# Kernel tuning notes

Measured on AMD Instinct MI355X. Metric: run time of the kernel, lower is better.

Reference implementation:

```python
import jax, jax.numpy as jnp
import numpy as np

EMB = 1024
HEAD = 64

def setup_inputs() -> dict:
    key = jax.random.key(0)
    kx, kq, kk, kv = jax.random.split(key, 4)
    x = jax.random.normal(kx, (8, 2048, EMB), dtype=jnp.float32)
    # nn.Linear(emb, head, bias=False): y = x @ W.T, W: [head, emb]. Store as [emb, head].
    s = 1.0 / np.sqrt(EMB)
    Wq = jax.random.uniform(kq, (EMB, HEAD), jnp.float32, -s, s)
    Wk = jax.random.uniform(kk, (EMB, HEAD), jnp.float32, -s, s)
    Wv = jax.random.uniform(kv, (EMB, HEAD), jnp.float32, -s, s)
    return {"x": x, "Wq": Wq, "Wk": Wk, "Wv": Wv}

def reference(x, Wq, Wk, Wv):
    B, T, C = x.shape
    q = x @ Wq  # [B,T,H]
    k = x @ Wk
    v = x @ Wv
    # NOTE: original scales by emb_size C, not head_size.
    wei = jnp.einsum('bth,bsh->bts', q, k) / jnp.sqrt(jnp.asarray(C, x.dtype))
    causal = jnp.tril(jnp.ones((T, T), dtype=bool))
    wei = jnp.where(causal, wei, -jnp.inf)
    wei = jax.nn.softmax(wei, axis=-1)
    return jnp.einsum('bts,bsh->bth', wei, v)
```

## Files before the change

kernel.cpp:

```cpp
#include <hip/hip_runtime.h>
#include <hip/hip_bf16.h>

typedef __bf16 bf16_t;
typedef __bf16 bf16x8 __attribute__((ext_vector_type(8)));
typedef __bf16 bf16x4 __attribute__((ext_vector_type(4)));
typedef float  f32x4  __attribute__((ext_vector_type(4)));

#define MFMA_BF16(A, B, C) __builtin_amdgcn_mfma_f32_16x16x32_bf16((A), (B), (C), 0, 0, 0)

#define BATCH 8
#define SEQ   2048
#define EMB   1024
#define HEAD  64

typedef __attribute__((address_space(3))) void as3_void;
typedef const __attribute__((address_space(1))) void as1_void;
#define GLOAD_LDS16(g, l) \
  __builtin_amdgcn_global_load_lds((as1_void*)(g), (as3_void*)(l), 16, 0, 0)

__global__ __launch_bounds__(256) void wtrans_kernel(
    const float* __restrict__ Wq, const float* __restrict__ Wk,
    const float* __restrict__ Wv, bf16_t* __restrict__ WT)
{
  __shared__ float tile[64][65];
  const int m  = blockIdx.x >> 4;
  const int kt = blockIdx.x & 15;
  const float* W = (m == 0) ? Wq : (m == 1) ? Wk : Wv;
  const float scale = (m == 0) ? 0.03125f : 1.0f;
  const int k0 = kt * 64;

  #pragma unroll
  for (int i = 0; i < 16; ++i) {
    int idx = i * 256 + threadIdx.x;
    int kk = idx >> 6, n = idx & 63;
    tile[kk][n] = W[(size_t)(k0 + kk) * HEAD + n];
  }
  __syncthreads();
  #pragma unroll
  for (int i = 0; i < 16; ++i) {
    int idx = i * 256 + threadIdx.x;
    int n = idx >> 6, kk = idx & 63;
    WT[((size_t)m * HEAD + n) * EMB + k0 + kk] = (bf16_t)(tile[kk][n] * scale);
  }
}

#define A_BYTES 8192
#define B_BYTES 12288
#define BUF_BYTES 20480

__global__ __launch_bounds__(256, 2) void qkv_kernel(
    const float* __restrict__ x, const bf16_t* __restrict__ WT,
    bf16_t* __restrict__ qo, bf16_t* __restrict__ ko, bf16_t* __restrict__ vT)
{
  __shared__ char lds[4 * BUF_BYTES];

  const int tid  = threadIdx.x;
  const int lane = tid & 63;
  const int wave = tid >> 6;
  const int l15 = lane & 15, l4 = lane >> 4;
  const int wm = wave >> 1, wn = wave & 1;
  const int rowbase = blockIdx.x * 64;

  const int a_row_sub = lane >> 3;
  const int a_src_off = (((lane & 7) ^ a_row_sub) << 4);
  const int b_row_sub = lane >> 2;
  const int b_src_off = (lane & 3) * 16;

  const int aswz = (l15 & 7) << 4;

  f32x4 acc[2][6];
  #pragma unroll
  for (int m = 0; m < 2; ++m)
    #pragma unroll
    for (int n = 0; n < 6; ++n) acc[m][n] = (f32x4){0.f, 0.f, 0.f, 0.f};

#define STAGE(t)                                                               \
  {                                                                            \
    char* buf = lds + ((t) & 3) * BUF_BYTES;                                   \
    _Pragma("unroll")                                                          \
    for (int j = 0; j < 2; ++j) {                                              \
      const int g = wave * 2 + j;                                              \
      const int row = 8 * g + a_row_sub;                                       \
      const char* src = (const char*)x + (size_t)(rowbase + row) * 4096        \
                        + (size_t)(t) * 128 + a_src_off;                       \
      GLOAD_LDS16(src, buf + g * 1024);                                        \
    }                                                                          \
    _Pragma("unroll")                                                          \
    for (int j = 0; j < 3; ++j) {                                              \
      const int g = wave * 3 + j;                                              \
      const int row = 16 * g + b_row_sub;                                      \
      const char* src = (const char*)WT + (size_t)row * 2048                   \
                        + (size_t)(t) * 64 + b_src_off;                        \
      GLOAD_LDS16(src, buf + A_BYTES + g * 1024);                              \
    }                                                                          \
  }

#define COMPUTE(t)                                                             \
  {                                                                            \
    const char* Ab = lds + ((t) & 3) * BUF_BYTES;                              \
    const char* Bb = Ab + A_BYTES;                                             \
    bf16x8 afr[2];                                                             \
    _Pragma("unroll")                                                          \
    for (int m = 0; m < 2; ++m) {                                              \
      const int R = wm * 32 + m * 16 + l15;                                    \
      f32x4 p0 = *(const f32x4*)(Ab + R * 128 + ((l4 * 32) ^ aswz));           \
      f32x4 p1 = *(const f32x4*)(Ab + R * 128 + ((l4 * 32 + 16) ^ aswz));      \
      bf16x8 a;                                                                \
      a[0] = (bf16_t)p0.x; a[1] = (bf16_t)p0.y;                                \
      a[2] = (bf16_t)p0.z; a[3] = (bf16_t)p0.w;                                \
      a[4] = (bf16_t)p1.x; a[5] = (bf16_t)p1.y;                                \
      a[6] = (bf16_t)p1.z; a[7] = (bf16_t)p1.w;                                \
      afr[m] = a;                                                              \
    }                                                                          \
    _Pragma("unroll")                                                          \
    for (int n = 0; n < 6; ++n) {                                              \
      const int R = wn * 96 + n * 16 + l15;                                    \
      bf16x8 b = *(const bf16x8*)(Bb + R * 64 + l4 * 16);                      \
      acc[0][n] = MFMA_BF16(afr[0], b, acc[0][n]);                             \
      acc[1][n] = MFMA_BF16(afr[1], b, acc[1][n]);                             \
    }                                                                          \
  }

  STAGE(0); STAGE(1); STAGE(2);
  asm volatile("s_waitcnt vmcnt(10)" ::: "memory");
  __builtin_amdgcn_s_barrier();

  #pragma unroll 4
  for (int t = 0; t < 28; ++t) {
    COMPUTE(t);
    STAGE(t + 3);
    asm volatile("s_waitcnt vmcnt(10)" ::: "memory");
    __builtin_amdgcn_s_barrier();
  }
  COMPUTE(28); STAGE(31);
  asm volatile("s_waitcnt vmcnt(10)" ::: "memory");
  __builtin_amdgcn_s_barrier();
  COMPUTE(29);
  asm volatile("s_waitcnt vmcnt(5)" ::: "memory");
  __builtin_amdgcn_s_barrier();
  COMPUTE(30);
  asm volatile("s_waitcnt vmcnt(0)" ::: "memory");
  __builtin_amdgcn_s_barrier();
  COMPUTE(31);
#undef STAGE
#undef COMPUTE

  #pragma unroll
  for (int n = 0; n < 6; ++n) {
    const int col = wn * 96 + n * 16;
    #pragma unroll
    for (int m = 0; m < 2; ++m) {
      const int r0 = rowbase + wm * 32 + m * 16 + l4 * 4;
      if (col < 64) {
        #pragma unroll
        for (int i = 0; i < 4; ++i)
          qo[(size_t)(r0 + i) * HEAD + col + l15] = (bf16_t)acc[m][n][i];
      } else if (col < 128) {
        #pragma unroll
        for (int i = 0; i < 4; ++i)
          ko[(size_t)(r0 + i) * HEAD + col - 64 + l15] = (bf16_t)acc[m][n][i];
      } else {
        const int h = col - 128 + l15;
        bf16x4 pk;
        #pragma unroll
        for (int i = 0; i < 4; ++i) pk[i] = (bf16_t)acc[m][n][i];
        *(bf16x4*)(vT + ((size_t)(r0 >> 11) * HEAD + h) * SEQ + (r0 & 2047)) = pk;
      }
    }
  }
}

__global__ __launch_bounds__(512, 4) void attn_kernel(
    const bf16_t* __restrict__ q, const bf16_t* __restrict__ k,
    const bf16_t* __restrict__ vT, float* __restrict__ out)
{
  __shared__ bf16_t P[8][16][72];
  __shared__ float olds[8][16][68];
  __shared__ float lsums[8][16];
  const int lane = threadIdx.x & 63;
  const int wave = threadIdx.x >> 6;
  const int l15 = lane & 15, l4 = lane >> 4;
  const int batch = blockIdx.x & 7;
  const int pair  = blockIdx.x >> 3;
  const int strip = (wave < 4) ? pair : (127 - pair);
  const int wsub  = wave & 3;
  const int qrow  = strip * 16;

  const bf16_t* qb = q  + ((size_t)batch * SEQ + qrow) * HEAD;
  const bf16_t* kb = k  + (size_t)batch * SEQ * HEAD;
  const bf16_t* vb = vT + (size_t)batch * HEAD * SEQ;

  bf16x8 aq0 = *(const bf16x8*)(qb + (size_t)l15 * HEAD + l4 * 8);
  bf16x8 aq1 = *(const bf16x8*)(qb + (size_t)l15 * HEAD + 32 + l4 * 8);

  f32x4 o[4];
  #pragma unroll
  for (int i = 0; i < 4; ++i) o[i] = (f32x4){0.f, 0.f, 0.f, 0.f};
  float lsum[4] = {0.f, 0.f, 0.f, 0.f};

  const int ntiles = (qrow >> 6) + 1;
  for (int t = wsub; t < ntiles; t += 4) {
    const int kv0 = t * 64;

    bf16x8 v0[4], v1[4];
    #pragma unroll
    for (int nf = 0; nf < 4; ++nf) {
      const bf16_t* vp = vb + (size_t)(nf * 16 + l15) * SEQ + kv0 + l4 * 8;
      v0[nf] = *(const bf16x8*)vp;
      v1[nf] = *(const bf16x8*)(vp + 32);
    }

    f32x4 s[4];
    #pragma unroll
    for (int nf = 0; nf < 4; ++nf) s[nf] = (f32x4){0.f, 0.f, 0.f, 0.f};
    __builtin_amdgcn_s_setprio(1);
    #pragma unroll
    for (int nf = 0; nf < 4; ++nf) {
      const bf16_t* kp = kb + (size_t)(kv0 + nf * 16 + l15) * HEAD + l4 * 8;
      bf16x8 b0 = *(const bf16x8*)kp;
      bf16x8 b1 = *(const bf16x8*)(kp + 32);
      s[nf] = MFMA_BF16(aq0, b0, s[nf]);
      s[nf] = MFMA_BF16(aq1, b1, s[nf]);
    }
    __builtin_amdgcn_s_setprio(0);

    const bool diag = (t == ntiles - 1);
    #pragma unroll
    for (int nf = 0; nf < 4; ++nf) {
      #pragma unroll
      for (int i = 0; i < 4; ++i) {
        float e = __expf(s[nf][i]);
        if (diag) {
          const int col = kv0 + nf * 16 + l15;
          const int row = qrow + l4 * 4 + i;
          e = (col <= row) ? e : 0.f;
        }
        lsum[i] += e;
        P[wave][l4 * 4 + i][nf * 16 + l15] = (bf16_t)e;
      }
    }
    asm volatile("s_waitcnt lgkmcnt(0)" ::: "memory");

    bf16x8 ap0 = *(const bf16x8*)&P[wave][l15][l4 * 8];
    bf16x8 ap1 = *(const bf16x8*)&P[wave][l15][32 + l4 * 8];
    __builtin_amdgcn_s_setprio(1);
    #pragma unroll
    for (int nf = 0; nf < 4; ++nf) {
      o[nf] = MFMA_BF16(ap0, v0[nf], o[nf]);
      o[nf] = MFMA_BF16(ap1, v1[nf], o[nf]);
    }
    __builtin_amdgcn_s_setprio(0);
  }

  #pragma unroll
  for (int i = 0; i < 4; ++i) {
    float v = lsum[i];
    v += __shfl_xor(v, 1);
    v += __shfl_xor(v, 2);
    v += __shfl_xor(v, 4);
    v += __shfl_xor(v, 8);
    if (l15 == 0) lsums[wave][l4 * 4 + i] = v;
  }
  #pragma unroll
  for (int nf = 0; nf < 4; ++nf)
    #pragma unroll
    for (int i = 0; i < 4; ++i)
      olds[wave][l4 * 4 + i][nf * 16 + l15] = o[nf][i];
  __syncthreads();

  {
    const int g  = threadIdx.x >> 8;
    const int tt = threadIdx.x & 255;
    const int r = tt >> 4, c0 = tt & 15;
    const int sstrip = g ? (127 - pair) : pair;
    const int w0 = g * 4;
    const float s = lsums[w0][r] + lsums[w0+1][r] + lsums[w0+2][r] + lsums[w0+3][r];
    const float rinv = 1.0f / s;
    float* ob = out + ((size_t)batch * SEQ + sstrip * 16 + r) * HEAD;
    #pragma unroll
    for (int j = 0; j < 4; ++j) {
      const int c = c0 + 16 * j;
      float v = olds[w0][r][c] + olds[w0+1][r][c] + olds[w0+2][r][c] + olds[w0+3][r][c];
      ob[c] = v * rinv;
    }
  }
}

extern "C" void kernel_launch(void* const* d_in, const int* in_sizes, int n_in,
                              void* d_out, int out_size, void* d_ws, size_t ws_size,
                              hipStream_t stream)
{
  const float* x  = (const float*)d_in[0];
  const float* Wq = (const float*)d_in[1];
  const float* Wk = (const float*)d_in[2];
  const float* Wv = (const float*)d_in[3];
  float* out = (float*)d_out;

  const size_t SZ_QKV = (size_t)BATCH * SEQ * HEAD * sizeof(bf16_t);
  if (ws_size < 3 * SZ_QKV + (size_t)192 * EMB * sizeof(bf16_t)) return;
  char* ws = (char*)d_ws;
  bf16_t* qo = (bf16_t*)(ws);
  bf16_t* ko = (bf16_t*)(ws + SZ_QKV);
  bf16_t* vT = (bf16_t*)(ws + 2 * SZ_QKV);
  bf16_t* WT = (bf16_t*)(ws + 3 * SZ_QKV);

  wtrans_kernel<<<dim3(48),  dim3(256), 0, stream>>>(Wq, Wk, Wv, WT);
  qkv_kernel  <<<dim3(256), dim3(256), 0, stream>>>(x, WT, qo, ko, vT);
  attn_kernel <<<dim3(512), dim3(512), 0, stream>>>(qo, ko, vT, out);
}
```

Before: 56.81 us.

## Halve QKV row tile and balance attention KV tiles across all eight waves

The QKV projection now uses 32-row blocks launched as 512 blocks, with each wave owning 48 output columns, so more blocks are available to fill the CUs. The attention kernel pools the KV tiles of the paired short and long strips and deals them round-robin to all eight waves, replacing the fixed four waves per strip. This balances work inside the block at the cost of two reduction passes. The Q scale now folds in log2(e) so exp2f replaces __expf, V loads are moved after the softmax, and attention launch bounds drop to 2 blocks per SIMD minimum.

New measurement: 64.96 us. 14.4% more time.

```diff
diff --git a/kernel.cpp b/kernel.cpp
--- a/kernel.cpp
+++ b/kernel.cpp
@@ -26,7 +26,7 @@
   const int m  = blockIdx.x >> 4;
   const int kt = blockIdx.x & 15;
   const float* W = (m == 0) ? Wq : (m == 1) ? Wk : Wv;
-  const float scale = (m == 0) ? 0.03125f : 1.0f;
+  const float scale = (m == 0) ? 0.045084219f : 1.0f;
   const int k0 = kt * 64;
 
   #pragma unroll
@@ -44,9 +44,9 @@
   }
 }
 
-#define A_BYTES 8192
+#define A_BYTES 4096
 #define B_BYTES 12288
-#define BUF_BYTES 20480
+#define BUF_BYTES 16384
 
 __global__ __launch_bounds__(256, 2) void qkv_kernel(
     const float* __restrict__ x, const bf16_t* __restrict__ WT,
@@ -58,8 +58,7 @@
   const int lane = tid & 63;
   const int wave = tid >> 6;
   const int l15 = lane & 15, l4 = lane >> 4;
-  const int wm = wave >> 1, wn = wave & 1;
-  const int rowbase = blockIdx.x * 64;
+  const int rowbase = blockIdx.x * 32;
 
   const int a_row_sub = lane >> 3;
   const int a_src_off = (((lane & 7) ^ a_row_sub) << 4);
@@ -68,22 +67,20 @@
 
   const int aswz = (l15 & 7) << 4;
 
-  f32x4 acc[2][6];
+  f32x4 acc[2][3];
   #pragma unroll
   for (int m = 0; m < 2; ++m)
     #pragma unroll
-    for (int n = 0; n < 6; ++n) acc[m][n] = (f32x4){0.f, 0.f, 0.f, 0.f};
+    for (int n = 0; n < 3; ++n) acc[m][n] = (f32x4){0.f, 0.f, 0.f, 0.f};
 
 #define STAGE(t)                                                               \
   {                                                                            \
     char* buf = lds + ((t) & 3) * BUF_BYTES;                                   \
-    _Pragma("unroll")                                                          \
-    for (int j = 0; j < 2; ++j) {                                              \
-      const int g = wave * 2 + j;                                              \
-      const int row = 8 * g + a_row_sub;                                       \
+    {                                                                          \
+      const int row = 8 * wave + a_row_sub;                                    \
       const char* src = (const char*)x + (size_t)(rowbase + row) * 4096        \
                         + (size_t)(t) * 128 + a_src_off;                       \
-      GLOAD_LDS16(src, buf + g * 1024);                                        \
+      GLOAD_LDS16(src, buf + wave * 1024);                                     \
     }                                                                          \
     _Pragma("unroll")                                                          \
     for (int j = 0; j < 3; ++j) {                                              \
@@ -102,7 +99,7 @@
     bf16x8 afr[2];                                                             \
     _Pragma("unroll")                                                          \
     for (int m = 0; m < 2; ++m) {                                              \
-      const int R = wm * 32 + m * 16 + l15;                                    \
+      const int R = m * 16 + l15;                                              \
       f32x4 p0 = *(const f32x4*)(Ab + R * 128 + ((l4 * 32) ^ aswz));           \
       f32x4 p1 = *(const f32x4*)(Ab + R * 128 + ((l4 * 32 + 16) ^ aswz));      \
       bf16x8 a;                                                                \
@@ -113,8 +110,8 @@
       afr[m] = a;                                                              \
     }                                                                          \
     _Pragma("unroll")                                                          \
-    for (int n = 0; n < 6; ++n) {                                              \
-      const int R = wn * 96 + n * 16 + l15;                                    \
+    for (int n = 0; n < 3; ++n) {                                              \
+      const int R = wave * 48 + n * 16 + l15;                                  \
       bf16x8 b = *(const bf16x8*)(Bb + R * 64 + l4 * 16);                      \
       acc[0][n] = MFMA_BF16(afr[0], b, acc[0][n]);                             \
       acc[1][n] = MFMA_BF16(afr[1], b, acc[1][n]);                             \
@@ -122,21 +119,18 @@
   }
 
   STAGE(0); STAGE(1); STAGE(2);
-  asm volatile("s_waitcnt vmcnt(10)" ::: "memory");
+  asm volatile("s_waitcnt vmcnt(8)" ::: "memory");
   __builtin_amdgcn_s_barrier();
 
   #pragma unroll 4
-  for (int t = 0; t < 28; ++t) {
+  for (int t = 0; t < 29; ++t) {
     COMPUTE(t);
     STAGE(t + 3);
-    asm volatile("s_waitcnt vmcnt(10)" ::: "memory");
+    asm volatile("s_waitcnt vmcnt(8)" ::: "memory");
     __builtin_amdgcn_s_barrier();
   }
-  COMPUTE(28); STAGE(31);
-  asm volatile("s_waitcnt vmcnt(10)" ::: "memory");
-  __builtin_amdgcn_s_barrier();
   COMPUTE(29);
-  asm volatile("s_waitcnt vmcnt(5)" ::: "memory");
+  asm volatile("s_waitcnt vmcnt(4)" ::: "memory");
   __builtin_amdgcn_s_barrier();
   COMPUTE(30);
   asm volatile("s_waitcnt vmcnt(0)" ::: "memory");
@@ -146,11 +140,11 @@
 #undef COMPUTE
 
   #pragma unroll
-  for (int n = 0; n < 6; ++n) {
-    const int col = wn * 96 + n * 16;
+  for (int n = 0; n < 3; ++n) {
+    const int col = wave * 48 + n * 16;
     #pragma unroll
     for (int m = 0; m < 2; ++m) {
-      const int r0 = rowbase + wm * 32 + m * 16 + l4 * 4;
+      const int r0 = rowbase + m * 16 + l4 * 4;
       if (col < 64) {
         #pragma unroll
         for (int i = 0; i < 4; ++i)
@@ -170,7 +164,7 @@
   }
 }
 
-__global__ __launch_bounds__(512, 4) void attn_kernel(
+__global__ __launch_bounds__(512, 2) void attn_kernel(
     const bf16_t* __restrict__ q, const bf16_t* __restrict__ k,
     const bf16_t* __restrict__ vT, float* __restrict__ out)
 {
@@ -182,33 +176,38 @@
   const int l15 = lane & 15, l4 = lane >> 4;
   const int batch = blockIdx.x & 7;
   const int pair  = blockIdx.x >> 3;
-  const int strip = (wave < 4) ? pair : (127 - pair);
-  const int wsub  = wave & 3;
-  const int qrow  = strip * 16;
-
-  const bf16_t* qb = q  + ((size_t)batch * SEQ + qrow) * HEAD;
+  const int stripA = pair, stripB = 127 - pair;
+  const int nA = (stripA >> 2) + 1;
+  const int nB = (stripB >> 2) + 1;
+  const int ntot = nA + nB;
+
   const bf16_t* kb = k  + (size_t)batch * SEQ * HEAD;
   const bf16_t* vb = vT + (size_t)batch * HEAD * SEQ;
-
-  bf16x8 aq0 = *(const bf16x8*)(qb + (size_t)l15 * HEAD + l4 * 8);
-  bf16x8 aq1 = *(const bf16x8*)(qb + (size_t)l15 * HEAD + 32 + l4 * 8);
-
-  f32x4 o[4];
-  #pragma unroll
-  for (int i = 0; i < 4; ++i) o[i] = (f32x4){0.f, 0.f, 0.f, 0.f};
-  float lsum[4] = {0.f, 0.f, 0.f, 0.f};
-
-  const int ntiles = (qrow >> 6) + 1;
-  for (int t = wsub; t < ntiles; t += 4) {
-    const int kv0 = t * 64;
-
-    bf16x8 v0[4], v1[4];
-    #pragma unroll
-    for (int nf = 0; nf < 4; ++nf) {
-      const bf16_t* vp = vb + (size_t)(nf * 16 + l15) * SEQ + kv0 + l4 * 8;
-      v0[nf] = *(const bf16x8*)vp;
-      v1[nf] = *(const bf16x8*)(vp + 32);
-    }
+  const bf16_t* qbA = q + ((size_t)batch * SEQ + stripA * 16) * HEAD;
+  const bf16_t* qbB = q + ((size_t)batch * SEQ + stripB * 16) * HEAD;
+
+  const bf16x8 aqA0 = *(const bf16x8*)(qbA + (size_t)l15 * HEAD + l4 * 8);
+  const bf16x8 aqA1 = *(const bf16x8*)(qbA + (size_t)l15 * HEAD + 32 + l4 * 8);
+  const bf16x8 aqB0 = *(const bf16x8*)(qbB + (size_t)l15 * HEAD + l4 * 8);
+  const bf16x8 aqB1 = *(const bf16x8*)(qbB + (size_t)l15 * HEAD + 32 + l4 * 8);
+
+  f32x4 oA[4], oB[4];
+  #pragma unroll
+  for (int i = 0; i < 4; ++i) {
+    oA[i] = (f32x4){0.f, 0.f, 0.f, 0.f};
+    oB[i] = (f32x4){0.f, 0.f, 0.f, 0.f};
+  }
+  float lsA[4] = {0.f, 0.f, 0.f, 0.f};
+  float lsB[4] = {0.f, 0.f, 0.f, 0.f};
+
+  for (int i = wave; i < ntot; i += 8) {
+    const bool isA = (i < nA);
+    const int tile = isA ? i : (i - nA);
+    const int nS   = isA ? nA : nB;
+    const int qrow = (isA ? stripA : stripB) * 16;
+    const int kv0  = tile * 64;
+    const bf16x8 aq0 = isA ? aqA0 : aqB0;
+    const bf16x8 aq1 = isA ? aqA1 : aqB1;
 
     f32x4 s[4];
     #pragma unroll
@@ -224,65 +223,91 @@
     }
     __builtin_amdgcn_s_setprio(0);
 
-    const bool diag = (t == ntiles - 1);
+    const bool diag = (tile == nS - 1);
+    float tsum[4] = {0.f, 0.f, 0.f, 0.f};
     #pragma unroll
     for (int nf = 0; nf < 4; ++nf) {
       #pragma unroll
-      for (int i = 0; i < 4; ++i) {
-        float e = __expf(s[nf][i]);
+      for (int i2 = 0; i2 < 4; ++i2) {
+        float e = exp2f(s[nf][i2]);
         if (diag) {
           const int col = kv0 + nf * 16 + l15;
-          const int row = qrow + l4 * 4 + i;
+          const int row = qrow + l4 * 4 + i2;
           e = (col <= row) ? e : 0.f;
         }
-        lsum[i] += e;
-        P[wave][l4 * 4 + i][nf * 16 + l15] = (bf16_t)e;
-      }
+        tsum[i2] += e;
+        P[wave][l4 * 4 + i2][nf * 16 + l15] = (bf16_t)e;
+      }
+    }
+
+    bf16x8 v0[4], v1[4];
+    #pragma unroll
+    for (int nf = 0; nf < 4; ++nf) {
+      const bf16_t* vp = vb + (size_t)(nf * 16 + l15) * SEQ + kv0 + l4 * 8;
+      v0[nf] = *(const bf16x8*)vp;
+      v1[nf] = *(const bf16x8*)(vp + 32);
     }
     asm volatile("s_waitcnt lgkmcnt(0)" ::: "memory");
 
     bf16x8 ap0 = *(const bf16x8*)&P[wave][l15][l4 * 8];
     bf16x8 ap1 = *(const bf16x8*)&P[wave][l15][32 + l4 * 8];
     __builtin_amdgcn_s_setprio(1);
-    #pragma unroll
-    for (int nf = 0; nf < 4; ++nf) {
-      o[nf] = MFMA_BF16(ap0, v0[nf], o[nf]);
-      o[nf] = MFMA_BF16(ap1, v1[nf], o[nf]);
+    if (isA) {
+      #pragma unroll
+      for (int nf = 0; nf < 4; ++nf) {
+        oA[nf] = MFMA_BF16(ap0, v0[nf], oA[nf]);
+        oA[nf] = MFMA_BF16(ap1, v1[nf], oA[nf]);
+      }
+      #pragma unroll
+      for (int i2 = 0; i2 < 4; ++i2) lsA[i2] += tsum[i2];
+    } else {
+      #pragma unroll
+      for (int nf = 0; nf < 4; ++nf) {
+        oB[nf] = MFMA_BF16(ap0, v0[nf], oB[nf]);
+        oB[nf] = MFMA_BF16(ap1, v1[nf], oB[nf]);
+      }
+      #pragma unroll
+      for (int i2 = 0; i2 < 4; ++i2) lsB[i2] += tsum[i2];
     }
     __builtin_amdgcn_s_setprio(0);
   }
 
   #pragma unroll
-  for (int i = 0; i < 4; ++i) {
-    float v = lsum[i];
-    v += __shfl_xor(v, 1);
-    v += __shfl_xor(v, 2);
-    v += __shfl_xor(v, 4);
-    v += __shfl_xor(v, 8);
-    if (l15 == 0) lsums[wave][l4 * 4 + i] = v;
-  }
-  #pragma unroll
-  for (int nf = 0; nf < 4; ++nf)
-    #pragma unroll
-    for (int i = 0; i < 4; ++i)
-      olds[wave][l4 * 4 + i][nf * 16 + l15] = o[nf][i];
-  __syncthreads();
-
-  {
-    const int g  = threadIdx.x >> 8;
-    const int tt = threadIdx.x & 255;
-    const int r = tt >> 4, c0 = tt & 15;
-    const int sstrip = g ? (127 - pair) : pair;
-    const int w0 = g * 4;
-    const float s = lsums[w0][r] + lsums[w0+1][r] + lsums[w0+2][r] + lsums[w0+3][r];
-    const float rinv = 1.0f / s;
-    float* ob = out + ((size_t)batch * SEQ + sstrip * 16 + r) * HEAD;
-    #pragma unroll
-    for (int j = 0; j < 4; ++j) {
-      const int c = c0 + 16 * j;
-      float v = olds[w0][r][c] + olds[w0+1][r][c] + olds[w0+2][r][c] + olds[w0+3][r][c];
-      ob[c] = v * rinv;
-    }
+  for (int pass = 0; pass < 2; ++pass) {
+    #pragma unroll
+    for (int i = 0; i < 4; ++i) {
+      float v = pass == 0 ? lsA[i] : lsB[i];
+      v += __shfl_xor(v, 1);
+      v += __shfl_xor(v, 2);
+      v += __shfl_xor(v, 4);
+      v += __shfl_xor(v, 8);
+      if (l15 == 0) lsums[wave][l4 * 4 + i] = v;
+    }
+    #pragma unroll
+    for (int nf = 0; nf < 4; ++nf)
+      #pragma unroll
+      for (int i = 0; i < 4; ++i)
+        olds[wave][l4 * 4 + i][nf * 16 + l15] = pass == 0 ? oA[nf][i] : oB[nf][i];
+    __syncthreads();
+
+    if (threadIdx.x < 256) {
+      const int r = threadIdx.x >> 4, c0 = threadIdx.x & 15;
+      float sum = 0.f;
+      #pragma unroll
+      for (int w = 0; w < 8; ++w) sum += lsums[w][r];
+      const float rinv = 1.0f / sum;
+      const int strip = pass == 0 ? stripA : stripB;
+      float* ob = out + ((size_t)batch * SEQ + strip * 16 + r) * HEAD;
+      #pragma unroll
+      for (int j = 0; j < 4; ++j) {
+        const int c = c0 + 16 * j;
+        float v = 0.f;
+        #pragma unroll
+        for (int w = 0; w < 8; ++w) v += olds[w][r][c];
+        ob[c] = v * rinv;
+      }
+    }
+    __syncthreads();
   }
 }
 
@@ -305,6 +330,6 @@
   bf16_t* WT = (bf16_t*)(ws + 3 * SZ_QKV);
 
   wtrans_kernel<<<dim3(48),  dim3(256), 0, stream>>>(Wq, Wk, Wv, WT);
-  qkv_kernel  <<<dim3(256), dim3(256), 0, stream>>>(x, WT, qo, ko, vT);
+  qkv_kernel  <<<dim3(512), dim3(256), 0, stream>>>(x, WT, qo, ko, vT);
   attn_kernel <<<dim3(512), dim3(512), 0, stream>>>(qo, ko, vT, out);
 }
```
